# Performance work log

Measured on AMD Instinct MI355X. Metric: run time of the kernel, lower is better.

The kernel has to match this reference:

```python
import jax, jax.numpy as jnp
import numpy as np

N = 100000
E = 640000
IN_CH = 64
HID = 128
HEADS = [4, 4, 1]
BN_EPS = 1e-5
NEG_SLOPE = 0.2  # GATConv default leaky relu slope


def setup_inputs() -> dict:
    key = jax.random.key(0)
    ks = iter(jax.random.split(key, 48))
    nrm = lambda shape, s=0.1: jax.random.normal(next(ks), shape, jnp.float32) * s
    return dict(
        x=jax.random.normal(next(ks), (N, IN_CH), jnp.float32),
        edge_index=jax.random.randint(next(ks), (2, E), 0, N),
        edge_weight=jax.random.uniform(next(ks), (E,), jnp.float32),
        Wproj=nrm((IN_CH, HID)), bproj=jnp.zeros((HID,), jnp.float32),
        gat_W=nrm((3, HID, HID)), att_src=nrm((3, HID)), att_dst=nrm((3, HID)),
        att_edge=nrm((3, HID)), lin_edge_W=nrm((3, HID)),
        gat_bias=jnp.zeros((3, HID), jnp.float32),
        bn_gamma=jnp.ones((3, HID), jnp.float32), bn_beta=jnp.zeros((3, HID), jnp.float32),
        bn_mean=nrm((3, HID), 0.05),
        bn_var=jax.random.uniform(next(ks), (3, HID), jnp.float32, 0.5, 1.5),
        ew_W1=nrm((3, 32)), ew_b1=jnp.zeros((3, 32), jnp.float32),
        ew_W2=nrm((3, 32)), ew_b2=jnp.zeros((3,), jnp.float32),
        symptom_attention=jnp.ones((HID,), jnp.float32),
        clf_W1=nrm((HID, 64)), clf_b1=jnp.zeros((64,), jnp.float32),
        clf_bn_gamma=jnp.ones((64,), jnp.float32), clf_bn_beta=jnp.zeros((64,), jnp.float32),
        clf_bn_mean=nrm((64,), 0.05),
        clf_bn_var=jax.random.uniform(next(ks), (64,), jnp.float32, 0.5, 1.5),
        clf_W2=nrm((64, 32)), clf_b2=jnp.zeros((32,), jnp.float32),
        clf_W3=nrm((32, 2)), clf_b3=jnp.zeros((2,), jnp.float32),
    )


def _bn(x, g, b, m, v):
    # eval-mode BatchNorm with running stats
    return (x - m) * jax.lax.rsqrt(v + BN_EPS) * g + b


def reference(x, edge_index, edge_weight, Wproj, bproj, gat_W, att_src, att_dst,
              att_edge, lin_edge_W, gat_bias, bn_gamma, bn_beta, bn_mean, bn_var,
              ew_W1, ew_b1, ew_W2, ew_b2, symptom_attention, clf_W1, clf_b1,
              clf_bn_gamma, clf_bn_beta, clf_bn_mean, clf_bn_var, clf_W2, clf_b2,
              clf_W3, clf_b3):
    n = x.shape[0]
    loop = jnp.arange(n)
    src = jnp.concatenate([edge_index[0], loop])  # [E+N] self loops appended
    dst = jnp.concatenate([edge_index[1], loop])
    h = x @ Wproj + bproj  # input projection -> [N, HID]
    for i, H in enumerate(HEADS):
        C = HID // H
        # edge attention MLP: Linear(1,32)->ReLU->Linear(32,1)->Sigmoid on raw edge_weight
        eh = jax.nn.relu(edge_weight[:, None] * ew_W1[i][None, :] + ew_b1[i])
        ea = jax.nn.sigmoid(eh @ ew_W2[i] + ew_b2[i])  # [E]
        few = edge_weight * ea  # final edge weight [E]
        # self-loop edge attr fill_value='mean'
        e_attr = jnp.concatenate([few, jnp.broadcast_to(jnp.mean(few), (n,))])  # [E+N]
        # GATConv
        xl = (h @ gat_W[i]).reshape(n, H, C)
        a_src = jnp.sum(xl * att_src[i].reshape(H, C), axis=-1)  # [N,H]
        a_dst = jnp.sum(xl * att_dst[i].reshape(H, C), axis=-1)  # [N,H]
        e_lin = (e_attr[:, None] * lin_edge_W[i][None, :]).reshape(-1, H, C)
        a_edge = jnp.sum(e_lin * att_edge[i].reshape(H, C), axis=-1)  # [E+N,H]
        alpha = jax.nn.leaky_relu(a_src[src] + a_dst[dst] + a_edge, NEG_SLOPE)
        amax = jax.ops.segment_max(alpha, dst, num_segments=n)
        ex = jnp.exp(alpha - amax[dst])
        denom = jax.ops.segment_sum(ex, dst, num_segments=n)
        w = ex / (denom[dst] + 1e-16)  # segment softmax over incoming edges
        out = jax.ops.segment_sum(w[:, :, None] * xl[src], dst, num_segments=n)
        h = out.reshape(n, HID) + gat_bias[i]
        h = jax.nn.elu(_bn(h, bn_gamma[i], bn_beta[i], bn_mean[i], bn_var[i]))
        # dropout is identity in eval mode
    h = h * symptom_attention
    c = jax.nn.relu(h @ clf_W1 + clf_b1)
    c = _bn(c, clf_bn_gamma, clf_bn_beta, clf_bn_mean, clf_bn_var)
    c = jax.nn.relu(c @ clf_W2 + clf_b2)
    logits = c @ clf_W3 + clf_b3
    return logits
```

## Files before the change

### kernel.cpp

```cpp
#include <hip/hip_runtime.h>
#include <hip/hip_fp16.h>
#include <math.h>

#define NN 100000
#define EE 640000
#define ENL (EE + NN)
#define HIDD 128

constexpr float BN_EPS = 1e-5f;

template<int KDIM, int NC, int EPI, int H>
__global__ __launch_bounds__(256) void k_gemm(
    const float* __restrict__ A, const float* __restrict__ W,
    const float* __restrict__ bias, float* __restrict__ out, int nrows,
    const float* __restrict__ att_s, const float* __restrict__ att_d,
    float* __restrict__ a_src, float* __restrict__ a_dst,
    const float* __restrict__ bng, const float* __restrict__ bnb,
    const float* __restrict__ bnm, const float* __restrict__ bnv)
{
    constexpr int TXN = NC / 4;
    constexpr int TYN = 256 / TXN;
    constexpr int RPT = 64 / TYN;
    __shared__ float Al[64][36];
    __shared__ float Wl[32][NC];
    const int t = threadIdx.x;
    const int tx = t % TXN, ty = t / TXN;
    const long rowBase = (long)blockIdx.x * 64;
    float acc[RPT][4];
#pragma unroll
    for (int r = 0; r < RPT; ++r) { acc[r][0]=0.f; acc[r][1]=0.f; acc[r][2]=0.f; acc[r][3]=0.f; }

    for (int kk = 0; kk < KDIM; kk += 32) {
#pragma unroll
        for (int j = 0; j < 2; ++j) {
            int idx = t + j * 256;
            int r = idx >> 3;
            int k4 = (idx & 7) << 2;
            long gr = rowBase + r;
            float4 v = make_float4(0.f, 0.f, 0.f, 0.f);
            if (gr < nrows) v = *(const float4*)(A + gr * KDIM + kk + k4);
            *(float4*)&Al[r][k4] = v;
        }
        constexpr int WLOAD = (32 * NC / 4) / 256;
#pragma unroll
        for (int j = 0; j < WLOAD; ++j) {
            int idx = t + j * 256;
            int k = idx / TXN;
            int c4 = (idx % TXN) << 2;
            *(float4*)&Wl[k][c4] = *(const float4*)(W + (long)(kk + k) * NC + c4);
        }
        __syncthreads();
#pragma unroll
        for (int k = 0; k < 32; ++k) {
            float4 wv = *(float4*)&Wl[k][tx * 4];
#pragma unroll
            for (int r = 0; r < RPT; ++r) {
                float av = Al[ty * RPT + r][k];
                acc[r][0] = fmaf(av, wv.x, acc[r][0]);
                acc[r][1] = fmaf(av, wv.y, acc[r][1]);
                acc[r][2] = fmaf(av, wv.z, acc[r][2]);
                acc[r][3] = fmaf(av, wv.w, acc[r][3]);
            }
        }
        __syncthreads();
    }

    const int col0 = tx * 4;
    if constexpr (EPI == 0) {
        float4 b4 = *(const float4*)(bias + col0);
#pragma unroll
        for (int r = 0; r < RPT; ++r) {
            long row = rowBase + ty * RPT + r;
            if (row < nrows) {
                float4 o = make_float4(acc[r][0] + b4.x, acc[r][1] + b4.y,
                                       acc[r][2] + b4.z, acc[r][3] + b4.w);
                *(float4*)(out + row * NC + col0) = o;
            }
        }
    } else if constexpr (EPI == 1) {
        __half* outh = reinterpret_cast<__half*>(out);
        float as4[4], ad4[4];
#pragma unroll
        for (int c = 0; c < 4; ++c) { as4[c] = att_s[col0 + c]; ad4[c] = att_d[col0 + c]; }
        constexpr int G = TXN / H;
#pragma unroll
        for (int r = 0; r < RPT; ++r) {
            long row = rowBase + ty * RPT + r;
            if (row < nrows) {
                union { __half2 h2[2]; uint2 u; } pk;
                pk.h2[0] = __floats2half2_rn(acc[r][0], acc[r][1]);
                pk.h2[1] = __floats2half2_rn(acc[r][2], acc[r][3]);
                *(uint2*)(outh + row * NC + col0) = pk.u;
            }
            float ps = 0.f, pd = 0.f;
#pragma unroll
            for (int c = 0; c < 4; ++c) {
                ps = fmaf(acc[r][c], as4[c], ps);
                pd = fmaf(acc[r][c], ad4[c], pd);
            }
#pragma unroll
            for (int m_ = 1; m_ < G; m_ <<= 1) {
                ps += __shfl_xor(ps, m_, 64);
                pd += __shfl_xor(pd, m_, 64);
            }
            if ((tx & (G - 1)) == 0 && row < nrows) {
                int h = tx / G;
                a_src[row * H + h] = ps;
                a_dst[row * H + h] = pd;
            }
        }
    } else {
        float4 b4 = *(const float4*)(bias + col0);
        float4 g4 = *(const float4*)(bng + col0);
        float4 be4 = *(const float4*)(bnb + col0);
        float4 m4 = *(const float4*)(bnm + col0);
        float4 v4 = *(const float4*)(bnv + col0);
        float s0 = rsqrtf(v4.x + BN_EPS) * g4.x;
        float s1 = rsqrtf(v4.y + BN_EPS) * g4.y;
        float s2 = rsqrtf(v4.z + BN_EPS) * g4.z;
        float s3 = rsqrtf(v4.w + BN_EPS) * g4.w;
#pragma unroll
        for (int r = 0; r < RPT; ++r) {
            long row = rowBase + ty * RPT + r;
            if (row < nrows) {
                float o0 = fmaxf(acc[r][0] + b4.x, 0.f);
                float o1 = fmaxf(acc[r][1] + b4.y, 0.f);
                float o2 = fmaxf(acc[r][2] + b4.z, 0.f);
                float o3 = fmaxf(acc[r][3] + b4.w, 0.f);
                float4 o = make_float4((o0 - m4.x) * s0 + be4.x,
                                       (o1 - m4.y) * s1 + be4.y,
                                       (o2 - m4.z) * s2 + be4.z,
                                       (o3 - m4.w) * s3 + be4.w);
                *(float4*)(out + row * NC + col0) = o;
            }
        }
    }
}

__global__ void k_prep(const float* __restrict__ lew, const float* __restrict__ ae,
                       float* __restrict__ scal, int H)
{
    __shared__ float p[128];
    int t = threadIdx.x;
    p[t] = lew[t] * ae[t];
    __syncthreads();
    if (t == 0) scal[0] = 0.f;
    if (t < H) {
        int Cc = 128 / H;
        float s = 0.f;
        for (int c = 0; c < Cc; ++c) s += p[t * Cc + c];
        scal[4 + t] = s;
    }
}

__global__ __launch_bounds__(256) void k_edgemlp(
    const float* __restrict__ ew, const float* __restrict__ W1,
    const float* __restrict__ b1, const float* __restrict__ W2,
    const float* __restrict__ b2, float* __restrict__ few,
    float* __restrict__ sumfew)
{
    __shared__ float red[4];
    int e = blockIdx.x * 256 + threadIdx.x;
    float f = 0.f;
    if (e < EE) {
        float w = ew[e];
        float acc = b2[0];
#pragma unroll
        for (int j = 0; j < 32; ++j) {
            float t_ = fmaf(w, W1[j], b1[j]);
            t_ = fmaxf(t_, 0.f);
            acc = fmaf(t_, W2[j], acc);
        }
        f = w / (1.f + __expf(-acc));
        few[e] = f;
    }
    float s = f;
#pragma unroll
    for (int m_ = 1; m_ < 64; m_ <<= 1) s += __shfl_xor(s, m_, 64);
    int lane = threadIdx.x & 63, wid = threadIdx.x >> 6;
    if (lane == 0) red[wid] = s;
    __syncthreads();
    if (threadIdx.x == 0) atomicAdd(sumfew, red[0] + red[1] + red[2] + red[3]);
}

__global__ __launch_bounds__(256) void k_hist(const int* __restrict__ edst, int* __restrict__ cnt)
{
    int e = blockIdx.x * 256 + threadIdx.x;
    if (e < ENL) {
        int d = (e < EE) ? edst[e] : (e - EE);
        atomicAdd(&cnt[d], 1);
    }
}

__global__ __launch_bounds__(256) void k_scan1(const int* __restrict__ cnt,
                                               int* __restrict__ tmp, int* __restrict__ part)
{
    __shared__ int s1[256];
    int t = threadIdx.x;
    int i = blockIdx.x * 256 + t;
    int x = (i < NN) ? cnt[i] : 0;
    s1[t] = x;
    __syncthreads();
#pragma unroll
    for (int off = 1; off < 256; off <<= 1) {
        int v_ = (t >= off) ? s1[t - off] : 0;
        __syncthreads();
        s1[t] += v_;
        __syncthreads();
    }
    if (i < NN) tmp[i] = s1[t] - x;
    if (t == 255) part[blockIdx.x] = s1[255];
}

__global__ void k_scan2(int* __restrict__ part, int nb)
{
    __shared__ int s1[512];
    int t = threadIdx.x;
    int x = (t < nb) ? part[t] : 0;
    s1[t] = x;
    __syncthreads();
#pragma unroll
    for (int off = 1; off < 512; off <<= 1) {
        int v_ = (t >= off) ? s1[t - off] : 0;
        __syncthreads();
        s1[t] += v_;
        __syncthreads();
    }
    if (t < nb) part[t] = s1[t] - x;
}

__global__ __launch_bounds__(256) void k_scan3(int* __restrict__ rp, int* __restrict__ cur,
                                               const int* __restrict__ part)
{
    int i = blockIdx.x * 256 + threadIdx.x;
    if (i < NN) {
        int v_ = rp[i] + part[blockIdx.x];
        rp[i] = v_;
        cur[i] = v_;
    } else if (i == NN) {
        rp[NN] = ENL;
    }
}

__global__ __launch_bounds__(256) void k_scatter(const int* __restrict__ edst,
                                                 int* __restrict__ cur, int* __restrict__ eid)
{
    int e = blockIdx.x * 256 + threadIdx.x;
    if (e < ENL) {
        int d = (e < EE) ? edst[e] : (e - EE);
        int pos = atomicAdd(&cur[d], 1);
        eid[pos] = e;
    }
}

__global__ __launch_bounds__(256) void k_psrc(const int* __restrict__ eid,
                                              const int* __restrict__ esrc,
                                              int* __restrict__ ssrc)
{
    int p = blockIdx.x * 256 + threadIdx.x;
    if (p < ENL) {
        int e = eid[p];
        ssrc[p] = (e < EE) ? esrc[e] : (e - EE);
    }
}

__global__ __launch_bounds__(256) void k_pfew(const int* __restrict__ eid,
                                              const float* __restrict__ few,
                                              const float* __restrict__ scal,
                                              float* __restrict__ sfew)
{
    int p = blockIdx.x * 256 + threadIdx.x;
    if (p < ENL) {
        int e = eid[p];
        sfew[p] = (e < EE) ? few[e] : scal[0] * (1.0f / EE);
    }
}

template<int H>
__global__ __launch_bounds__(256) void k_agg(
    const __half* __restrict__ xl, const float* __restrict__ a_src,
    const float* __restrict__ a_dst, const float* __restrict__ sfew,
    const int* __restrict__ ssrc, const float* __restrict__ scal,
    const int* __restrict__ rp,
    const float* __restrict__ bias, const float* __restrict__ bng,
    const float* __restrict__ bnb, const float* __restrict__ bnm,
    const float* __restrict__ bnv, float* __restrict__ hout)
{
    __shared__ float lw[4][H][66];
    const int lane = threadIdx.x & 63;
    const int wid  = threadIdx.x >> 6;
    const int n = (blockIdx.x << 2) + wid;
    float Kc[H], adn[H];
#pragma unroll
    for (int h = 0; h < H; ++h) { Kc[h] = scal[4 + h]; adn[h] = a_dst[n * H + h]; }
    const int p0 = rp[n];
    const int deg = rp[n + 1] - p0;
    const bool fast = (deg <= 64);

    float acc0 = 0.f, acc1 = 0.f;

    if (fast) {
        const bool act = lane < deg;
        float al[H];
        if (act) {
            int s = ssrc[p0 + lane];
            float ea = sfew[p0 + lane];
            if constexpr (H == 4) {
                float4 as = *(const float4*)(a_src + s * 4);
                float x0 = as.x + adn[0] + ea * Kc[0];
                float x1 = as.y + adn[1] + ea * Kc[1];
                float x2 = as.z + adn[2] + ea * Kc[2];
                float x3 = as.w + adn[3] + ea * Kc[3];
                al[0] = (x0 > 0.f) ? x0 : 0.2f * x0;
                al[1] = (x1 > 0.f) ? x1 : 0.2f * x1;
                al[2] = (x2 > 0.f) ? x2 : 0.2f * x2;
                al[3] = (x3 > 0.f) ? x3 : 0.2f * x3;
            } else {
                float x0 = a_src[s] + adn[0] + ea * Kc[0];
                al[0] = (x0 > 0.f) ? x0 : 0.2f * x0;
            }
        } else {
#pragma unroll
            for (int h = 0; h < H; ++h) al[h] = -INFINITY;
        }
        float mx[H], ex[H], dn[H];
#pragma unroll
        for (int h = 0; h < H; ++h) {
            mx[h] = al[h];
#pragma unroll
            for (int m_ = 1; m_ < 64; m_ <<= 1) mx[h] = fmaxf(mx[h], __shfl_xor(mx[h], m_, 64));
        }
#pragma unroll
        for (int h = 0; h < H; ++h) {
            ex[h] = act ? __expf(al[h] - mx[h]) : 0.f;
            dn[h] = ex[h];
#pragma unroll
            for (int m_ = 1; m_ < 64; m_ <<= 1) dn[h] += __shfl_xor(dn[h], m_, 64);
            lw[wid][h][lane] = ex[h] * (1.0f / (dn[h] + 1e-16f));
        }
    }
    __syncthreads();

    if (fast) {
        const int myh = (H == 4) ? (lane >> 4) : 0;
        const float* wrow = &lw[wid][myh][0];
        int j = 0;
        for (; j + 4 <= deg; j += 4) {
            int s0 = ssrc[p0 + j + 0];
            int s1 = ssrc[p0 + j + 1];
            int s2 = ssrc[p0 + j + 2];
            int s3 = ssrc[p0 + j + 3];
            float w0 = wrow[j + 0], w1 = wrow[j + 1], w2 = wrow[j + 2], w3 = wrow[j + 3];
            float2 f0 = __half22float2(((const __half2*)(xl + (size_t)s0 * HIDD))[lane]);
            float2 f1 = __half22float2(((const __half2*)(xl + (size_t)s1 * HIDD))[lane]);
            float2 f2 = __half22float2(((const __half2*)(xl + (size_t)s2 * HIDD))[lane]);
            float2 f3 = __half22float2(((const __half2*)(xl + (size_t)s3 * HIDD))[lane]);
            acc0 = fmaf(w0, f0.x, acc0); acc1 = fmaf(w0, f0.y, acc1);
            acc0 = fmaf(w1, f1.x, acc0); acc1 = fmaf(w1, f1.y, acc1);
            acc0 = fmaf(w2, f2.x, acc0); acc1 = fmaf(w2, f2.y, acc1);
            acc0 = fmaf(w3, f3.x, acc0); acc1 = fmaf(w3, f3.y, acc1);
        }
        for (; j < deg; ++j) {
            int s0 = ssrc[p0 + j];
            float w0 = wrow[j];
            float2 f0 = __half22float2(((const __half2*)(xl + (size_t)s0 * HIDD))[lane]);
            acc0 = fmaf(w0, f0.x, acc0); acc1 = fmaf(w0, f0.y, acc1);
        }
    } else {
        float mx[H], dn[H];
#pragma unroll
        for (int h = 0; h < H; ++h) mx[h] = -INFINITY;
        for (int base = 0; base < deg; base += 64) {
            int j = base + lane;
            if (j < deg) {
                int s = ssrc[p0 + j];
                float ea = sfew[p0 + j];
#pragma unroll
                for (int h = 0; h < H; ++h) {
                    float x_ = a_src[s * H + h] + adn[h] + ea * Kc[h];
                    x_ = (x_ > 0.f) ? x_ : 0.2f * x_;
                    mx[h] = fmaxf(mx[h], x_);
                }
            }
        }
#pragma unroll
        for (int h = 0; h < H; ++h) {
#pragma unroll
            for (int m_ = 1; m_ < 64; m_ <<= 1) mx[h] = fmaxf(mx[h], __shfl_xor(mx[h], m_, 64));
            dn[h] = 0.f;
        }
        for (int base = 0; base < deg; base += 64) {
            int j = base + lane;
            if (j < deg) {
                int s = ssrc[p0 + j];
                float ea = sfew[p0 + j];
#pragma unroll
                for (int h = 0; h < H; ++h) {
                    float x_ = a_src[s * H + h] + adn[h] + ea * Kc[h];
                    x_ = (x_ > 0.f) ? x_ : 0.2f * x_;
                    dn[h] += __expf(x_ - mx[h]);
                }
            }
        }
#pragma unroll
        for (int h = 0; h < H; ++h) {
#pragma unroll
            for (int m_ = 1; m_ < 64; m_ <<= 1) dn[h] += __shfl_xor(dn[h], m_, 64);
            dn[h] = 1.0f / (dn[h] + 1e-16f);
        }
        for (int j = 0; j < deg; ++j) {
            int s = ssrc[p0 + j];
            float ea = sfew[p0 + j];
            float wsel;
            if constexpr (H == 4) {
                float4 as = *(const float4*)(a_src + s * 4);
                float x0 = as.x + adn[0] + ea * Kc[0]; x0 = (x0 > 0.f) ? x0 : 0.2f * x0;
                float x1 = as.y + adn[1] + ea * Kc[1]; x1 = (x1 > 0.f) ? x1 : 0.2f * x1;
                float x2 = as.z + adn[2] + ea * Kc[2]; x2 = (x2 > 0.f) ? x2 : 0.2f * x2;
                float x3 = as.w + adn[3] + ea * Kc[3]; x3 = (x3 > 0.f) ? x3 : 0.2f * x3;
                float w0 = __expf(x0 - mx[0]) * dn[0];
                float w1 = __expf(x1 - mx[1]) * dn[1];
                float w2 = __expf(x2 - mx[2]) * dn[2];
                float w3 = __expf(x3 - mx[3]) * dn[3];
                wsel = (lane < 16) ? w0 : ((lane < 32) ? w1 : ((lane < 48) ? w2 : w3));
            } else {
                float x0 = a_src[s] + adn[0] + ea * Kc[0]; x0 = (x0 > 0.f) ? x0 : 0.2f * x0;
                wsel = __expf(x0 - mx[0]) * dn[0];
            }
            float2 f = __half22float2(((const __half2*)(xl + (size_t)s * HIDD))[lane]);
            acc0 = fmaf(wsel, f.x, acc0);
            acc1 = fmaf(wsel, f.y, acc1);
        }
    }

    {
        int c0 = 2 * lane;
        float2 bi = *(const float2*)(bias + c0);
        float2 g  = *(const float2*)(bng + c0);
        float2 bb = *(const float2*)(bnb + c0);
        float2 mm = *(const float2*)(bnm + c0);
        float2 vv = *(const float2*)(bnv + c0);
        float o0 = acc0 + bi.x;
        o0 = (o0 - mm.x) * rsqrtf(vv.x + BN_EPS) * g.x + bb.x;
        o0 = (o0 > 0.f) ? o0 : (__expf(o0) - 1.f);
        float o1 = acc1 + bi.y;
        o1 = (o1 - mm.y) * rsqrtf(vv.y + BN_EPS) * g.y + bb.y;
        o1 = (o1 > 0.f) ? o1 : (__expf(o1) - 1.f);
        *(float2*)(hout + (size_t)n * HIDD + c0) = make_float2(o0, o1);
    }
}

__global__ void k_scaleW1(const float* __restrict__ W1, const float* __restrict__ sym,
                          float* __restrict__ W1s)
{
    int i = blockIdx.x * 256 + threadIdx.x;
    if (i < 128 * 64) W1s[i] = W1[i] * sym[i >> 6];
}

__global__ __launch_bounds__(256) void k_clf2(const float* __restrict__ c1,
                                              const float* __restrict__ W2,
                                              const float* __restrict__ b2,
                                              float* __restrict__ c2)
{
    __shared__ float Wl[64][32];
    int t = threadIdx.x;
#pragma unroll
    for (int j = 0; j < 2; ++j) {
        int idx = t + j * 256;
        ((float4*)Wl)[idx] = ((const float4*)W2)[idx];
    }
    __syncthreads();
    int n = blockIdx.x * 256 + t;
    if (n >= NN) return;
    float acc[32];
#pragma unroll
    for (int j = 0; j < 32; ++j) acc[j] = b2[j];
    const float* row = c1 + (long)n * 64;
#pragma unroll
    for (int k0 = 0; k0 < 64; k0 += 4) {
        float4 hv = *(const float4*)(row + k0);
#pragma unroll
        for (int kk = 0; kk < 4; ++kk) {
            float h_ = (&hv.x)[kk];
#pragma unroll
            for (int j4 = 0; j4 < 8; ++j4) {
                float4 w4 = *(float4*)&Wl[k0 + kk][j4 * 4];
                acc[j4 * 4 + 0] = fmaf(h_, w4.x, acc[j4 * 4 + 0]);
                acc[j4 * 4 + 1] = fmaf(h_, w4.y, acc[j4 * 4 + 1]);
                acc[j4 * 4 + 2] = fmaf(h_, w4.z, acc[j4 * 4 + 2]);
                acc[j4 * 4 + 3] = fmaf(h_, w4.w, acc[j4 * 4 + 3]);
            }
        }
    }
    float* o = c2 + (long)n * 32;
#pragma unroll
    for (int j4 = 0; j4 < 8; ++j4) {
        float4 v = make_float4(fmaxf(acc[j4 * 4 + 0], 0.f), fmaxf(acc[j4 * 4 + 1], 0.f),
                               fmaxf(acc[j4 * 4 + 2], 0.f), fmaxf(acc[j4 * 4 + 3], 0.f));
        *(float4*)(o + j4 * 4) = v;
    }
}

__global__ __launch_bounds__(256) void k_clf3(const float* __restrict__ c2,
                                              const float* __restrict__ W3,
                                              const float* __restrict__ b3,
                                              float* __restrict__ out)
{
    int n = blockIdx.x * 256 + threadIdx.x;
    if (n >= NN) return;
    const float* row = c2 + (long)n * 32;
    float l0 = b3[0], l1 = b3[1];
#pragma unroll
    for (int k = 0; k < 32; ++k) {
        float cv = row[k];
        l0 = fmaf(cv, W3[k * 2 + 0], l0);
        l1 = fmaf(cv, W3[k * 2 + 1], l1);
    }
    *(float2*)(out + (long)n * 2) = make_float2(l0, l1);
}

extern "C" void kernel_launch(void* const* d_in, const int* in_sizes, int n_in,
                              void* d_out, int out_size, void* d_ws, size_t ws_size,
                              hipStream_t stream)
{
    const float* x          = (const float*)d_in[0];
    const int*   edge_index = (const int*)d_in[1];
    const float* edge_w     = (const float*)d_in[2];
    const float* Wproj      = (const float*)d_in[3];
    const float* bproj      = (const float*)d_in[4];
    const float* gat_W      = (const float*)d_in[5];
    const float* att_src    = (const float*)d_in[6];
    const float* att_dst    = (const float*)d_in[7];
    const float* att_edge   = (const float*)d_in[8];
    const float* lin_edge_W = (const float*)d_in[9];
    const float* gat_bias   = (const float*)d_in[10];
    const float* bn_g       = (const float*)d_in[11];
    const float* bn_b       = (const float*)d_in[12];
    const float* bn_m       = (const float*)d_in[13];
    const float* bn_v       = (const float*)d_in[14];
    const float* ew_W1      = (const float*)d_in[15];
    const float* ew_b1      = (const float*)d_in[16];
    const float* ew_W2      = (const float*)d_in[17];
    const float* ew_b2      = (const float*)d_in[18];
    const float* sym        = (const float*)d_in[19];
    const float* clf_W1     = (const float*)d_in[20];
    const float* clf_b1     = (const float*)d_in[21];
    const float* clf_bng    = (const float*)d_in[22];
    const float* clf_bnb    = (const float*)d_in[23];
    const float* clf_bnm    = (const float*)d_in[24];
    const float* clf_bnv    = (const float*)d_in[25];
    const float* clf_W2     = (const float*)d_in[26];
    const float* clf_b2     = (const float*)d_in[27];
    const float* clf_W3     = (const float*)d_in[28];
    const float* clf_b3     = (const float*)d_in[29];
    float* outp = (float*)d_out;

    float* ws   = (float*)d_ws;
    float* hbuf = ws;
    float* xlf  = hbuf + 12800000;
    __half* xl  = (__half*)xlf;
    float* c1   = xlf;
    int*   ssrc = (int*)(xlf + 6400000);
    float* sfew = xlf + 7200000;
    float* c2   = xlf + 6400000;
    float* asrc = xlf + 12800000;
    float* adst = asrc + 400000;
    float* fewp = adst + 400000;
    float* scal = fewp + 640000;
    float* W1s  = scal + 16;
    int* rp   = (int*)(W1s + 8192);
    int* cur  = rp + 100004;
    int* eid  = cur + 100000;
    int* part = eid + 740000;

    const int* esrc = edge_index;
    const int* edst = edge_index + EE;

    hipMemsetAsync(cur, 0, NN * sizeof(int), stream);

    k_gemm<64, 128, 0, 1><<<1563, 256, 0, stream>>>(
        x, Wproj, bproj, hbuf, NN,
        nullptr, nullptr, nullptr, nullptr, nullptr, nullptr, nullptr, nullptr);

    k_hist<<<2891, 256, 0, stream>>>(edst, cur);
    k_scan1<<<391, 256, 0, stream>>>(cur, rp, part);
    k_scan2<<<1, 512, 0, stream>>>(part, 391);
    k_scan3<<<391, 256, 0, stream>>>(rp, cur, part);
    k_scatter<<<2891, 256, 0, stream>>>(edst, cur, eid);
    k_psrc<<<2891, 256, 0, stream>>>(eid, esrc, ssrc);

    for (int i = 0; i < 3; ++i) {
        int H = (i == 2) ? 1 : 4;
        k_prep<<<1, 128, 0, stream>>>(lin_edge_W + i * 128, att_edge + i * 128, scal, H);
        k_edgemlp<<<2500, 256, 0, stream>>>(edge_w, ew_W1 + i * 32, ew_b1 + i * 32,
                                            ew_W2 + i * 32, ew_b2 + i, fewp, scal);
        k_pfew<<<2891, 256, 0, stream>>>(eid, fewp, scal, sfew);
        if (H == 4) {
            k_gemm<128, 128, 1, 4><<<1563, 256, 0, stream>>>(
                hbuf, gat_W + i * 128 * 128, nullptr, xlf, NN,
                att_src + i * 128, att_dst + i * 128, asrc, adst,
                nullptr, nullptr, nullptr, nullptr);
            k_agg<4><<<25000, 256, 0, stream>>>(
                xl, asrc, adst, sfew, ssrc, scal, rp,
                gat_bias + i * 128, bn_g + i * 128, bn_b + i * 128,
                bn_m + i * 128, bn_v + i * 128, hbuf);
        } else {
            k_gemm<128, 128, 1, 1><<<1563, 256, 0, stream>>>(
                hbuf, gat_W + i * 128 * 128, nullptr, xlf, NN,
                att_src + i * 128, att_dst + i * 128, asrc, adst,
                nullptr, nullptr, nullptr, nullptr);
            k_agg<1><<<25000, 256, 0, stream>>>(
                xl, asrc, adst, sfew, ssrc, scal, rp,
                gat_bias + i * 128, bn_g + i * 128, bn_b + i * 128,
                bn_m + i * 128, bn_v + i * 128, hbuf);
        }
    }

    k_scaleW1<<<32, 256, 0, stream>>>(clf_W1, sym, W1s);
    k_gemm<128, 64, 2, 1><<<1563, 256, 0, stream>>>(
        hbuf, W1s, clf_b1, c1, NN,
        nullptr, nullptr, nullptr, nullptr, clf_bng, clf_bnb, clf_bnm, clf_bnv);
    k_clf2<<<391, 256, 0, stream>>>(c1, clf_W2, clf_b2, c2);
    k_clf3<<<391, 256, 0, stream>>>(c2, clf_W3, clf_b3, outp);
}
```

Before: 784.2 us.

## Use fp16 MFMA for GAT projection GEMM and split attention-score kernel

Replaces the fp32 FMA GEMM for the per-layer GAT projection with a new kernel using MFMA 16x16x32 f16 instructions on half-precision A and a transposed half weight. The attention dot products (a_src, a_dst) leave the GEMM epilogue and move to a separate k_att kernel that rereads the fp16 xl output. This targets GEMM compute cost at the price of an extra kernel launch, an extra pass over xl, and fp16 rounding of the inputs hbuf and W, which previously stayed fp32 inside the GEMM.

```diff
diff --git a/kernel.cpp b/kernel.cpp
--- a/kernel.cpp
+++ b/kernel.cpp
@@ -9,12 +9,13 @@
 
 constexpr float BN_EPS = 1e-5f;
 
-template<int KDIM, int NC, int EPI, int H>
+typedef _Float16 f16x8 __attribute__((ext_vector_type(8)));
+typedef float f32x4 __attribute__((ext_vector_type(4)));
+
+template<int KDIM, int NC, int EPI>
 __global__ __launch_bounds__(256) void k_gemm(
     const float* __restrict__ A, const float* __restrict__ W,
     const float* __restrict__ bias, float* __restrict__ out, int nrows,
-    const float* __restrict__ att_s, const float* __restrict__ att_d,
-    float* __restrict__ a_src, float* __restrict__ a_dst,
     const float* __restrict__ bng, const float* __restrict__ bnb,
     const float* __restrict__ bnm, const float* __restrict__ bnv)
 {
@@ -75,38 +76,6 @@
                 float4 o = make_float4(acc[r][0] + b4.x, acc[r][1] + b4.y,
                                        acc[r][2] + b4.z, acc[r][3] + b4.w);
                 *(float4*)(out + row * NC + col0) = o;
-            }
-        }
-    } else if constexpr (EPI == 1) {
-        __half* outh = reinterpret_cast<__half*>(out);
-        float as4[4], ad4[4];
-#pragma unroll
-        for (int c = 0; c < 4; ++c) { as4[c] = att_s[col0 + c]; ad4[c] = att_d[col0 + c]; }
-        constexpr int G = TXN / H;
-#pragma unroll
-        for (int r = 0; r < RPT; ++r) {
-            long row = rowBase + ty * RPT + r;
-            if (row < nrows) {
-                union { __half2 h2[2]; uint2 u; } pk;
-                pk.h2[0] = __floats2half2_rn(acc[r][0], acc[r][1]);
-                pk.h2[1] = __floats2half2_rn(acc[r][2], acc[r][3]);
-                *(uint2*)(outh + row * NC + col0) = pk.u;
-            }
-            float ps = 0.f, pd = 0.f;
-#pragma unroll
-            for (int c = 0; c < 4; ++c) {
-                ps = fmaf(acc[r][c], as4[c], ps);
-                pd = fmaf(acc[r][c], ad4[c], pd);
-            }
-#pragma unroll
-            for (int m_ = 1; m_ < G; m_ <<= 1) {
-                ps += __shfl_xor(ps, m_, 64);
-                pd += __shfl_xor(pd, m_, 64);
-            }
-            if ((tx & (G - 1)) == 0 && row < nrows) {
-                int h = tx / G;
-                a_src[row * H + h] = ps;
-                a_dst[row * H + h] = pd;
             }
         }
     } else {
@@ -135,6 +104,101 @@
             }
         }
     }
+}
+
+__global__ void k_prepW(const float* __restrict__ Wk, __half* __restrict__ Wt)
+{
+    int idx = blockIdx.x * 256 + threadIdx.x;
+    int k = idx >> 7, n = idx & 127;
+    Wt[n * 128 + k] = (__half)Wk[idx];
+}
+
+__global__ __launch_bounds__(256) void k_mgemm(
+    const float* __restrict__ A, const __half* __restrict__ Wt,
+    __half* __restrict__ xlh, int nrows)
+{
+    __shared__ _Float16 Ah[64][136];
+    __shared__ _Float16 Wl[128][136];
+    const int t = threadIdx.x;
+    const int lane = t & 63, w = t >> 6;
+    const long rowBase = (long)blockIdx.x * 64;
+
+#pragma unroll
+    for (int j = 0; j < 8; ++j) {
+        int flat = t + j * 256;
+        int r = flat >> 5;
+        int c4 = (flat & 31) << 2;
+        float4 v = make_float4(0.f, 0.f, 0.f, 0.f);
+        long gr = rowBase + r;
+        if (gr < nrows) v = *(const float4*)(A + gr * 128 + c4);
+        _Float16* dst = &Ah[r][c4];
+        dst[0] = (_Float16)v.x; dst[1] = (_Float16)v.y;
+        dst[2] = (_Float16)v.z; dst[3] = (_Float16)v.w;
+    }
+#pragma unroll
+    for (int j = 0; j < 8; ++j) {
+        int flat = t + j * 256;
+        int r = flat >> 4;
+        int ch = (flat & 15) << 3;
+        *(uint4*)&Wl[r][ch] = *(const uint4*)(Wt + r * 128 + ch);
+    }
+    __syncthreads();
+
+    const int row16 = lane & 15, kb = lane >> 4;
+    f32x4 acc[8];
+#pragma unroll
+    for (int cb = 0; cb < 8; ++cb) acc[cb] = (f32x4){0.f, 0.f, 0.f, 0.f};
+#pragma unroll
+    for (int ks = 0; ks < 4; ++ks) {
+        f16x8 a = *(const f16x8*)&Ah[w * 16 + row16][ks * 32 + kb * 8];
+#pragma unroll
+        for (int cb = 0; cb < 8; ++cb) {
+            f16x8 b = *(const f16x8*)&Wl[cb * 16 + row16][ks * 32 + kb * 8];
+            acc[cb] = __builtin_amdgcn_mfma_f32_16x16x32_f16(a, b, acc[cb], 0, 0, 0);
+        }
+    }
+
+    _Float16 (*Oh)[136] = Ah;
+#pragma unroll
+    for (int cb = 0; cb < 8; ++cb) {
+#pragma unroll
+        for (int r = 0; r < 4; ++r) {
+            Oh[w * 16 + kb * 4 + r][cb * 16 + row16] = (_Float16)acc[cb][r];
+        }
+    }
+    __syncthreads();
+#pragma unroll
+    for (int j = 0; j < 4; ++j) {
+        int flat = t + j * 256;
+        int r = flat >> 4;
+        int ch = (flat & 15) << 3;
+        long gr = rowBase + r;
+        if (gr < nrows) *(uint4*)(xlh + gr * 128 + ch) = *(const uint4*)&Oh[r][ch];
+    }
+}
+
+template<int H>
+__global__ __launch_bounds__(256) void k_att(
+    const __half* __restrict__ xlh, const float* __restrict__ att_s,
+    const float* __restrict__ att_d, float* __restrict__ asrc,
+    float* __restrict__ adst)
+{
+    int gid = blockIdx.x * 256 + threadIdx.x;
+    if (gid >= NN * H) return;
+    int row = gid / H, h = gid % H;
+    constexpr int C = 128 / H;
+    const __half* xr = xlh + (size_t)row * 128 + h * C;
+    const float* as = att_s + h * C;
+    const float* ad = att_d + h * C;
+    float ps = 0.f, pd = 0.f;
+#pragma unroll
+    for (int c = 0; c < C; c += 2) {
+        float2 f = __half22float2(*(const __half2*)(xr + c));
+        ps = fmaf(f.x, as[c], ps); ps = fmaf(f.y, as[c + 1], ps);
+        pd = fmaf(f.x, ad[c], pd); pd = fmaf(f.y, ad[c + 1], pd);
+    }
+    asrc[gid] = ps;
+    adst[gid] = pd;
 }
 
 __global__ void k_prep(const float* __restrict__ lew, const float* __restrict__ ae,
@@ -568,7 +632,8 @@
     float* fewp = adst + 400000;
     float* scal = fewp + 640000;
     float* W1s  = scal + 16;
-    int* rp   = (int*)(W1s + 8192);
+    __half* Wt_h = (__half*)(W1s + 8192);
+    int* rp   = (int*)(W1s + 8192 + 8192);
     int* cur  = rp + 100004;
     int* eid  = cur + 100000;
     int* part = eid + 740000;
@@ -578,9 +643,8 @@
 
     hipMemsetAsync(cur, 0, NN * sizeof(int), stream);
 
-    k_gemm<64, 128, 0, 1><<<1563, 256, 0, stream>>>(
-        x, Wproj, bproj, hbuf, NN,
-        nullptr, nullptr, nullptr, nullptr, nullptr, nullptr, nullptr, nullptr);
+    k_gemm<64, 128, 0><<<1563, 256, 0, stream>>>(
+        x, Wproj, bproj, hbuf, NN, nullptr, nullptr, nullptr, nullptr);
 
     k_hist<<<2891, 256, 0, stream>>>(edst, cur);
     k_scan1<<<391, 256, 0, stream>>>(cur, rp, part);
@@ -595,20 +659,18 @@
         k_edgemlp<<<2500, 256, 0, stream>>>(edge_w, ew_W1 + i * 32, ew_b1 + i * 32,
                                             ew_W2 + i * 32, ew_b2 + i, fewp, scal);
         k_pfew<<<2891, 256, 0, stream>>>(eid, fewp, scal, sfew);
+        k_prepW<<<64, 256, 0, stream>>>(gat_W + i * 128 * 128, Wt_h);
+        k_mgemm<<<1563, 256, 0, stream>>>(hbuf, Wt_h, xl, NN);
         if (H == 4) {
-            k_gemm<128, 128, 1, 4><<<1563, 256, 0, stream>>>(
-                hbuf, gat_W + i * 128 * 128, nullptr, xlf, NN,
-                att_src + i * 128, att_dst + i * 128, asrc, adst,
-                nullptr, nullptr, nullptr, nullptr);
+            k_att<4><<<1563, 256, 0, stream>>>(xl, att_src + i * 128, att_dst + i * 128,
+                                               asrc, adst);
             k_agg<4><<<25000, 256, 0, stream>>>(
                 xl, asrc, adst, sfew, ssrc, scal, rp,
                 gat_bias + i * 128, bn_g + i * 128, bn_b + i * 128,
                 bn_m + i * 128, bn_v + i * 128, hbuf);
         } else {
-            k_gemm<128, 128, 1, 1><<<1563, 256, 0, stream>>>(
-                hbuf, gat_W + i * 128 * 128, nullptr, xlf, NN,
-                att_src + i * 128, att_dst + i * 128, asrc, adst,
-                nullptr, nullptr, nullptr, nullptr);
+            k_att<1><<<391, 256, 0, stream>>>(xl, att_src + i * 128, att_dst + i * 128,
+                                              asrc, adst);
             k_agg<1><<<25000, 256, 0, stream>>>(
                 xl, asrc, adst, sfew, ssrc, scal, rp,
                 gat_bias + i * 128, bn_g + i * 128, bn_b + i * 128,
@@ -617,9 +679,8 @@
     }
 
     k_scaleW1<<<32, 256, 0, stream>>>(clf_W1, sym, W1s);
-    k_gemm<128, 64, 2, 1><<<1563, 256, 0, stream>>>(
-        hbuf, W1s, clf_b1, c1, NN,
-        nullptr, nullptr, nullptr, nullptr, clf_bng, clf_bnb, clf_bnm, clf_bnv);
+    k_gemm<128, 64, 2><<<1563, 256, 0, stream>>>(
+        hbuf, W1s, clf_b1, c1, NN, clf_bng, clf_bnb, clf_bnm, clf_bnv);
     k_clf2<<<391, 256, 0, stream>>>(c1, clf_W2, clf_b2, c2);
     k_clf3<<<391, 256, 0, stream>>>(c2, clf_W3, clf_b3, outp);
 }
```

New measurement: 737.6 us. 1.06x faster.
